# Kernel tuning notes

Hardware: AMD Instinct MI355X
Metric: run time of the kernel (lower is better)

The kernel has to match this reference:

```python
import jax, jax.numpy as jnp
import numpy as np
from jax import lax

EPS = 1e-5
DN = ('NCHW', 'OIHW', 'NCHW')


def batchnorm(x, gamma, beta):
    # training-mode BN: stats over (N, H, W)
    m = x.mean(axis=(0, 2, 3), keepdims=True)
    v = x.var(axis=(0, 2, 3), keepdims=True)
    g = gamma[None, :, None, None]
    b = beta[None, :, None, None]
    return (x - m) * (g / jnp.sqrt(v + EPS)) + b


def input_scale(x, stride):
    # channel mean -> 3x3 box filter (1/9 each), padding 1
    a = x.mean(axis=1, keepdims=True)  # [N,1,H,W]
    k = jnp.full((1, 1, 3, 3), 1.0 / 9.0, dtype=x.dtype)
    return lax.conv_general_dilated(a, k, (stride, stride), ((1, 1), (1, 1)),
                                    dimension_numbers=DN)


def binarize_ste(x):
    # sign with straight-through estimator (grad passes where |x|<=1)
    c = jnp.clip(x, -1.0, 1.0)
    return c + lax.stop_gradient(jnp.sign(x) - c)


def blconv(x, w, stride):
    # XNOR-style binarized conv: sign(x) * (sign(w)*mean|w| per out channel)
    bx = binarize_ste(x)
    alpha = jnp.abs(w).mean(axis=(1, 2, 3))  # [O]
    bw = jnp.sign(w) * alpha[:, None, None, None]
    return lax.conv_general_dilated(bx, bw, (stride, stride), ((1, 1), (1, 1)),
                                    dimension_numbers=DN)


def setup_inputs() -> dict:
    key = jax.random.key(0)
    ks = jax.random.split(key, 3)
    C = 256
    x = jax.random.normal(ks[0], (32, C, 56, 56), dtype=jnp.float32)
    w1 = jax.random.normal(ks[1], (C, C, 3, 3), dtype=jnp.float32) * 0.05
    w2 = jax.random.normal(ks[2], (C, C, 3, 3), dtype=jnp.float32) * 0.05
    bn1_gamma = jnp.ones((C,), jnp.float32)
    bn1_beta = jnp.zeros((C,), jnp.float32)
    bn2_gamma = jnp.ones((C,), jnp.float32)
    bn2_beta = jnp.zeros((C,), jnp.float32)
    return {"x": x, "bn1_gamma": bn1_gamma, "bn1_beta": bn1_beta, "w1": w1,
            "bn2_gamma": bn2_gamma, "bn2_beta": bn2_beta, "w2": w2}


def reference(x, bn1_gamma, bn1_beta, w1, bn2_gamma, bn2_beta, w2):
    stride = 1
    identity = x
    out = batchnorm(x, bn1_gamma, bn1_beta)
    K1 = input_scale(out, stride)
    out = blconv(out, w1, stride) * K1
    out = jax.nn.relu(out)
    out = batchnorm(out, bn2_gamma, bn2_beta)
    K2 = input_scale(out, 1)
    out = blconv(out, w2, 1) * K2
    out = out + identity
    return jax.nn.relu(out)
```

## Files before the change

kernel.cpp:

```cpp
#include <hip/hip_runtime.h>
#include <stdint.h>

#define NB 32
#define CC 256
#define HH 56
#define WW 56
#define PP (HH*WW)
#define NPIX (NB*PP)
#define W32 8
#define KEPS 1e-5f

__global__ void k_stats(const float* __restrict__ x, float* __restrict__ ssum, float* __restrict__ ssq) {
    int plane = blockIdx.x;
    int c = plane & (CC - 1);
    const float4* xp = (const float4*)(x + (size_t)plane * PP);
    float s = 0.f, q = 0.f;
    for (int i = threadIdx.x; i < PP / 4; i += blockDim.x) {
        float4 v = xp[i];
        s += v.x + v.y + v.z + v.w;
        q = fmaf(v.x, v.x, q); q = fmaf(v.y, v.y, q);
        q = fmaf(v.z, v.z, q); q = fmaf(v.w, v.w, q);
    }
#pragma unroll
    for (int off = 32; off; off >>= 1) { s += __shfl_down(s, off); q += __shfl_down(q, off); }
    __shared__ float ls[4], lq[4];
    int wv = threadIdx.x >> 6, ln = threadIdx.x & 63;
    if (ln == 0) { ls[wv] = s; lq[wv] = q; }
    __syncthreads();
    if (threadIdx.x == 0) {
        float S = 0.f, Q = 0.f;
        for (int w = 0; w < 4; ++w) { S += ls[w]; Q += lq[w]; }
        atomicAdd(&ssum[c], S); atomicAdd(&ssq[c], Q);
    }
}

__global__ void k_stats2(const short* __restrict__ ci, const float* __restrict__ alpha1,
                         const float* __restrict__ k1, float* __restrict__ ssum, float* __restrict__ ssq) {
    int plane = blockIdx.x;
    int o = plane & (CC - 1);
    int n = plane >> 8;
    const short4* cp = (const short4*)(ci + (size_t)plane * PP);
    const float4* kp = (const float4*)(k1 + (size_t)n * PP);
    float al = alpha1[o];
    float s = 0.f, q = 0.f;
    for (int i = threadIdx.x; i < PP / 4; i += blockDim.x) {
        short4 c4 = cp[i];
        float4 kf = kp[i];
        float v0 = fmaxf(al * kf.x * (float)c4.x, 0.f);
        float v1 = fmaxf(al * kf.y * (float)c4.y, 0.f);
        float v2 = fmaxf(al * kf.z * (float)c4.z, 0.f);
        float v3 = fmaxf(al * kf.w * (float)c4.w, 0.f);
        s += v0 + v1 + v2 + v3;
        q = fmaf(v0, v0, q); q = fmaf(v1, v1, q);
        q = fmaf(v2, v2, q); q = fmaf(v3, v3, q);
    }
#pragma unroll
    for (int off = 32; off; off >>= 1) { s += __shfl_down(s, off); q += __shfl_down(q, off); }
    __shared__ float ls[4], lq[4];
    int wv = threadIdx.x >> 6, ln = threadIdx.x & 63;
    if (ln == 0) { ls[wv] = s; lq[wv] = q; }
    __syncthreads();
    if (threadIdx.x == 0) {
        float S = 0.f, Q = 0.f;
        for (int w = 0; w < 4; ++w) { S += ls[w]; Q += lq[w]; }
        atomicAdd(&ssum[o], S); atomicAdd(&ssq[o], Q);
    }
}

__global__ void k_wprep(const float* __restrict__ w1, const float* __restrict__ w2,
                        uint32_t* __restrict__ wb1, uint32_t* __restrict__ wb2,
                        float* __restrict__ al1, float* __restrict__ al2,
                        int* __restrict__ adj1, int* __restrict__ adj2,
                        float* __restrict__ zstats) {
    int o2 = blockIdx.x;
    int lane = threadIdx.x;
    if (o2 < 16) zstats[o2 * 64 + lane] = 0.f;
    const float* w = (o2 < CC) ? w1 : w2;
    uint32_t* wb   = (o2 < CC) ? wb1 : wb2;
    float* al      = (o2 < CC) ? al1 : al2;
    int* adj       = (o2 < CC) ? adj1 : adj2;
    int o = o2 & (CC - 1);
    float asum = 0.f;
    int pt[9] = {0,0,0,0,0,0,0,0,0};
    for (int cg = 0; cg < 4; ++cg) {
        int c = cg * 64 + lane;
        const float* wp = w + ((size_t)o * CC + c) * 9;
        for (int t = 0; t < 9; ++t) {
            float wv = wp[t];
            asum += fabsf(wv);
            unsigned long long m = __ballot(wv >= 0.0f);
            pt[t] += __popcll(m);
            if (lane == 0) {
                wb[(t * CC + o) * W32 + cg * 2]     = (uint32_t)m;
                wb[(t * CC + o) * W32 + cg * 2 + 1] = (uint32_t)(m >> 32);
            }
        }
    }
#pragma unroll
    for (int off = 32; off; off >>= 1) asum += __shfl_down(asum, off);
    if (lane == 0) al[o] = asum * (1.0f / 2304.0f);
    if (lane < 9) {
        const unsigned vm[3] = {0u, 0x007u, 0x1C0u};
        const unsigned hm[3] = {0u, 0x049u, 0x124u};
        unsigned mask = vm[lane / 3] | hm[lane % 3];
        int nv = 9 - __popc(mask);
        int wsum = 0;
#pragma unroll
        for (int t = 0; t < 9; ++t) if ((mask >> t) & 1) wsum += pt[t];
        adj[o * 16 + lane] = 256 * nv + 2 * wsum;
    }
}

__global__ void k_bn1pack(const float* __restrict__ x,
                          const float* __restrict__ ssum, const float* __restrict__ ssq,
                          const float* __restrict__ gamma, const float* __restrict__ beta,
                          uint32_t* __restrict__ xbits, float* __restrict__ a) {
    __shared__ float sscale[CC], sbias[CC];
    {
        int t = threadIdx.x;
        float m   = ssum[t] * (1.0f / NPIX);
        float var = fmaf(-m, m, ssq[t] * (1.0f / NPIX));
        float sc  = gamma[t] / sqrtf(var + KEPS);
        sscale[t] = sc;
        sbias[t]  = fmaf(-m, sc, beta[t]);
    }
    __syncthreads();
    int lane = threadIdx.x & 63, wv = threadIdx.x >> 6;
    int n = blockIdx.x / 49;
    int pix = blockIdx.x * 64 + lane;
    int p = pix - n * PP;
    const float* xp = x + (size_t)n * CC * PP + p;
    uint32_t b0 = 0, b1 = 0;
    float asum = 0.f;
#pragma unroll
    for (int i = 0; i < 64; ++i) {
        int c = (wv << 6) + i;
        float v = xp[(size_t)c * PP];
        float bnv = fmaf(v, sscale[c], sbias[c]);
        asum += bnv;
        uint32_t bit = (bnv >= 0.0f) ? 1u : 0u;
        if (i < 32) b0 |= bit << i; else b1 |= bit << (i - 32);
    }
    ((uint2*)xbits)[(size_t)pix * 4 + wv] = make_uint2(b0, b1);
    __shared__ float lsum[4][64];
    lsum[wv][lane] = asum;
    __syncthreads();
    if (wv == 0)
        a[pix] = (lsum[0][lane] + lsum[1][lane] + lsum[2][lane] + lsum[3][lane]) * (1.0f / CC);
}

__global__ void k_bn2pack(const short* __restrict__ ci, const float* __restrict__ alpha1,
                          const float* __restrict__ k1,
                          const float* __restrict__ ssum, const float* __restrict__ ssq,
                          const float* __restrict__ gamma, const float* __restrict__ beta,
                          uint32_t* __restrict__ xbits, float* __restrict__ a) {
    __shared__ float sscale[CC], sbias[CC];
    {
        int t = threadIdx.x;
        float m   = ssum[t] * (1.0f / NPIX);
        float var = fmaf(-m, m, ssq[t] * (1.0f / NPIX));
        float sc  = gamma[t] / sqrtf(var + KEPS);
        sscale[t] = sc;
        sbias[t]  = fmaf(-m, sc, beta[t]);
    }
    __syncthreads();
    int lane = threadIdx.x & 63, wv = threadIdx.x >> 6;
    int n = blockIdx.x / 49;
    int pix = blockIdx.x * 64 + lane;
    int p = pix - n * PP;
    const short* cp = ci + (size_t)n * CC * PP + p;
    float kv = k1[pix];
    uint32_t b0 = 0, b1 = 0;
    float asum = 0.f;
#pragma unroll
    for (int i = 0; i < 64; ++i) {
        int o = (wv << 6) + i;
        float val = fmaxf(alpha1[o] * kv * (float)cp[(size_t)o * PP], 0.f);
        float bnv = fmaf(val, sscale[o], sbias[o]);
        asum += bnv;
        uint32_t bit = (bnv >= 0.0f) ? 1u : 0u;
        if (i < 32) b0 |= bit << i; else b1 |= bit << (i - 32);
    }
    ((uint2*)xbits)[(size_t)pix * 4 + wv] = make_uint2(b0, b1);
    __shared__ float lsum[4][64];
    lsum[wv][lane] = asum;
    __syncthreads();
    if (wv == 0)
        a[pix] = (lsum[0][lane] + lsum[1][lane] + lsum[2][lane] + lsum[3][lane]) * (1.0f / CC);
}

__global__ void k_box(const float* __restrict__ a, float* __restrict__ k) {
    int gid = blockIdx.x * 256 + threadIdx.x;
    int n = gid / PP;
    int p = gid - n * PP;
    int h = p / WW, w = p - (p / WW) * WW;
    const float* ap = a + (size_t)n * PP;
    float s = 0.f;
    for (int dr = -1; dr <= 1; ++dr) {
        int hh = h + dr;
        if (hh < 0 || hh >= HH) continue;
        for (int dc = -1; dc <= 1; ++dc) {
            int ww2 = w + dc;
            if (ww2 < 0 || ww2 >= WW) continue;
            s += ap[hh * WW + ww2];
        }
    }
    k[gid] = s * (1.0f / 9.0f);
}

template<bool FIRST>
__global__ __launch_bounds__(448, 8) void k_conv(
    const uint32_t* __restrict__ xbits, const uint32_t* __restrict__ wbits,
    const int* __restrict__ adj, const float* __restrict__ alpha,
    const float* __restrict__ amap, short* __restrict__ out_i16,
    const float* __restrict__ ident, float* __restrict__ outf)
{
    constexpr int TH = 8, TO = 16;
    constexpr int LW = 58;
    __shared__ uint32_t lds_x[(TH + 2) * LW * W32];

    int b = blockIdx.x;
    int ob = b & 15, hb = (b >> 4) % 7, n = b / 112;
    int h0 = hb * TH, o0 = ob * TO;
    int tid = threadIdx.x;

    for (int i = tid; i < (TH + 2) * LW * 2; i += 448) {
        int r = i / (LW * 2), j = i - r * (LW * 2);
        int c = j >> 1, half = j & 1;
        int gr = h0 - 1 + r, gc = c - 1;
        uint4 v = make_uint4(0u, 0u, 0u, 0u);
        if (gr >= 0 && gr < HH && gc >= 0 && gc < WW)
            v = ((const uint4*)(xbits + ((size_t)n * PP + (size_t)gr * WW + gc) * W32))[half];
        ((uint4*)lds_x)[i] = v;
    }
    __syncthreads();

    int row = tid / WW, col = tid - (tid / WW) * WW;
    int h = h0 + row;
    int vf = (h == 0) ? 1 : ((h == HH - 1) ? 2 : 0);
    int hf = (col == 0) ? 1 : ((col == WW - 1) ? 2 : 0);
    int type = vf * 3 + hf;

    float kv = 0.f;
    if (!FIRST) {
        const float* ap = amap + (size_t)n * PP;
        float s = 0.f;
        for (int dr = -1; dr <= 1; ++dr) {
            int hh = h + dr;
            if (hh < 0 || hh >= HH) continue;
            for (int dc2 = -1; dc2 <= 1; ++dc2) {
                int wc = col + dc2;
                if (wc < 0 || wc >= WW) continue;
                s += ap[hh * WW + wc];
            }
        }
        kv = s * (1.0f / 9.0f);
    }
    size_t obase = (size_t)n * CC * PP + (size_t)h * WW + col;

    int P[TO];
#pragma unroll
    for (int o = 0; o < TO; ++o) P[o] = 0;

#pragma unroll 1
    for (int dr = 0; dr < 3; ++dr) {
#pragma unroll 1
        for (int dc = 0; dc < 3; ++dc) {
            int base = ((row + dr) * LW + (col + dc)) * W32;
            uint4 xa = *(const uint4*)&lds_x[base];
            uint4 xb = *(const uint4*)&lds_x[base + 4];
            int t = dr * 3 + dc;
            const uint4* __restrict__ wq = (const uint4*)wbits + ((size_t)t * CC + o0) * 2;
#pragma unroll
            for (int o = 0; o < TO; ++o) {
                uint4 wa = wq[o * 2], wb2 = wq[o * 2 + 1];
                int P0 = P[o];
                P0 += __popc(xa.x ^ wa.x);
                P0 += __popc(xa.y ^ wa.y);
                P0 += __popc(xa.z ^ wa.z);
                P0 += __popc(xa.w ^ wa.w);
                P0 += __popc(xb.x ^ wb2.x);
                P0 += __popc(xb.y ^ wb2.y);
                P0 += __popc(xb.z ^ wb2.z);
                P0 += __popc(xb.w ^ wb2.w);
                P[o] = P0;
            }
        }
    }

#pragma unroll
    for (int o = 0; o < TO; ++o) {
        int oo = o0 + o;
        int acc = adj[oo * 16 + type] - 2 * P[o];
        size_t oidx = obase + (size_t)oo * PP;
        if (FIRST) {
            out_i16[oidx] = (short)acc;
        } else {
            float res = alpha[oo] * kv * (float)acc;
            outf[oidx] = fmaxf(res + ident[oidx], 0.f);
        }
    }
}

extern "C" void kernel_launch(void* const* d_in, const int* in_sizes, int n_in,
                              void* d_out, int out_size, void* d_ws, size_t ws_size,
                              hipStream_t stream)
{
    const float* x  = (const float*)d_in[0];
    const float* g1 = (const float*)d_in[1];
    const float* b1 = (const float*)d_in[2];
    const float* w1 = (const float*)d_in[3];
    const float* g2 = (const float*)d_in[4];
    const float* b2 = (const float*)d_in[5];
    const float* w2 = (const float*)d_in[6];
    float* out = (float*)d_out;

    char* ws = (char*)d_ws;
    float* s1sum  = (float*)(ws + 0);
    float* s1sq   = (float*)(ws + 1024);
    float* s2sum  = (float*)(ws + 2048);
    float* s2sq   = (float*)(ws + 3072);
    float* alpha1 = (float*)(ws + 8192);
    float* alpha2 = (float*)(ws + 9216);
    int*   adj1   = (int*)(ws + 10240);
    int*   adj2   = (int*)(ws + 26624);
    uint32_t* wbits1 = (uint32_t*)(ws + 43008);
    uint32_t* wbits2 = (uint32_t*)(ws + 116736);
    float* a1 = (float*)(ws + 190464);
    float* k1 = (float*)(ws + 591872);
    float* a2 = (float*)(ws + 993280);
    uint32_t* xbits1 = (uint32_t*)(ws + 1796096);
    uint32_t* xbits2 = (uint32_t*)(ws + 5007360);
    short* ci = (short*)(ws + 8218624);

    k_wprep<<<2 * CC, 64, 0, stream>>>(w1, w2, wbits1, wbits2, alpha1, alpha2, adj1, adj2, s1sum);
    k_stats<<<NB * CC, 256, 0, stream>>>(x, s1sum, s1sq);
    k_bn1pack<<<NPIX / 64, 256, 0, stream>>>(x, s1sum, s1sq, g1, b1, xbits1, a1);
    k_box<<<NPIX / 256, 256, 0, stream>>>(a1, k1);
    k_conv<true><<<NB * 7 * 16, 448, 0, stream>>>(xbits1, wbits1, adj1, nullptr, nullptr, ci, nullptr, nullptr);
    k_stats2<<<NB * CC, 256, 0, stream>>>(ci, alpha1, k1, s2sum, s2sq);
    k_bn2pack<<<NPIX / 64, 256, 0, stream>>>(ci, alpha1, k1, s2sum, s2sq, g2, b2, xbits2, a2);
    k_conv<false><<<NB * 7 * 16, 448, 0, stream>>>(xbits2, wbits2, adj2, alpha2, a2, nullptr, x, out);
}
```

Before: 538.3 us.

## Replace popcount binary conv with int8 MFMA convolution using ±1 byte encoding

Adds a new path that encodes binarized activations and weights as ±1 int8 bytes in channel-last layout and computes both 3x3 convolutions with 32x32x32 int8 MFMA instructions instead of XNOR/popcount with padding adjustments. The BN-pack kernels now write per-pixel channel-contiguous bytes through an LDS transpose. The second conv reads a precomputed box-filtered map (a new k_box pass) instead of computing it inline. The path is taken only when the workspace is large enough, otherwise the old popcount path runs. It trades 8x larger activation storage and traffic for matrix-core throughput.

```diff
diff --git a/kernel.cpp b/kernel.cpp
--- a/kernel.cpp
+++ b/kernel.cpp
@@ -9,6 +9,10 @@
 #define NPIX (NB*PP)
 #define W32 8
 #define KEPS 1e-5f
+
+typedef __attribute__((ext_vector_type(4)))  int i32x4;
+typedef __attribute__((ext_vector_type(16))) int i32x16;
+
 
 __global__ void k_stats(const float* __restrict__ x, float* __restrict__ ssum, float* __restrict__ ssq) {
     int plane = blockIdx.x;
@@ -67,11 +71,236 @@
     }
 }
 
-__global__ void k_wprep(const float* __restrict__ w1, const float* __restrict__ w2,
-                        uint32_t* __restrict__ wb1, uint32_t* __restrict__ wb2,
-                        float* __restrict__ al1, float* __restrict__ al2,
-                        int* __restrict__ adj1, int* __restrict__ adj2,
-                        float* __restrict__ zstats) {
+__global__ void k_box(const float* __restrict__ a, float* __restrict__ k) {
+    int gid = blockIdx.x * 256 + threadIdx.x;
+    int n = gid / PP;
+    int p = gid - n * PP;
+    int h = p / WW, w = p - (p / WW) * WW;
+    const float* ap = a + (size_t)n * PP;
+    float s = 0.f;
+    for (int dr = -1; dr <= 1; ++dr) {
+        int hh = h + dr;
+        if (hh < 0 || hh >= HH) continue;
+        for (int dc = -1; dc <= 1; ++dc) {
+            int ww2 = w + dc;
+            if (ww2 < 0 || ww2 >= WW) continue;
+            s += ap[hh * WW + ww2];
+        }
+    }
+    k[gid] = s * (1.0f / 9.0f);
+}
+
+__global__ void k_wprepM(const float* __restrict__ w1, const float* __restrict__ w2,
+                         uint8_t* __restrict__ wp1, uint8_t* __restrict__ wp2,
+                         float* __restrict__ al1, float* __restrict__ al2,
+                         float* __restrict__ zstats) {
+    int o2 = blockIdx.x;
+    int lane = threadIdx.x;
+    if (o2 < 16) zstats[o2 * 64 + lane] = 0.f;
+    const float* w = (o2 < CC) ? w1 : w2;
+    uint8_t* wp    = (o2 < CC) ? wp1 : wp2;
+    float* al      = (o2 < CC) ? al1 : al2;
+    int o = o2 & (CC - 1);
+    float asum = 0.f;
+    for (int cg = 0; cg < 4; ++cg) {
+        int c = cg * 64 + lane;
+        const float* wpt = w + ((size_t)o * CC + c) * 9;
+        int c32 = c >> 5;
+        int rem = c & 31;
+        for (int t = 0; t < 9; ++t) {
+            float wv = wpt[t];
+            asum += fabsf(wv);
+            int kg = t * 8 + c32;
+            wp[((size_t)kg * CC + o) * 32 + rem] = (wv >= 0.0f) ? (uint8_t)1 : (uint8_t)0xFF;
+        }
+    }
+#pragma unroll
+    for (int off = 32; off; off >>= 1) asum += __shfl_down(asum, off);
+    if (lane == 0) al[o] = asum * (1.0f / 2304.0f);
+}
+
+__global__ void k_bn1packM(const float* __restrict__ x,
+                           const float* __restrict__ ssum, const float* __restrict__ ssq,
+                           const float* __restrict__ gamma, const float* __restrict__ beta,
+                           uint8_t* __restrict__ xi8, float* __restrict__ a) {
+    __shared__ float sscale[CC], sbias[CC];
+    __shared__ uint32_t ldsT[64][68];
+    __shared__ float lsum[4][64];
+    int t = threadIdx.x;
+    {
+        float m   = ssum[t] * (1.0f / NPIX);
+        float var = fmaf(-m, m, ssq[t] * (1.0f / NPIX));
+        float sc  = gamma[t] / sqrtf(var + KEPS);
+        sscale[t] = sc;
+        sbias[t]  = fmaf(-m, sc, beta[t]);
+    }
+    __syncthreads();
+    int lane = t & 63, wv = t >> 6;
+    int n = blockIdx.x / 49;
+    int pix = blockIdx.x * 64 + lane;
+    int p = pix - n * PP;
+    const float* xp = x + (size_t)n * CC * PP + p;
+    float asum = 0.f;
+    for (int i4 = 0; i4 < 16; ++i4) {
+        uint32_t pk = 0;
+#pragma unroll
+        for (int u = 0; u < 4; ++u) {
+            int c = (wv << 6) + i4 * 4 + u;
+            float v = xp[(size_t)c * PP];
+            float bnv = fmaf(v, sscale[c], sbias[c]);
+            asum += bnv;
+            uint32_t byte = (bnv >= 0.0f) ? 0x01u : 0xFFu;
+            pk |= byte << (8 * u);
+        }
+        ldsT[lane][(wv << 4) + i4] = pk;
+    }
+    lsum[wv][lane] = asum;
+    __syncthreads();
+    if (wv == 0)
+        a[pix] = (lsum[0][lane] + lsum[1][lane] + lsum[2][lane] + lsum[3][lane]) * (1.0f / CC);
+    size_t gbase = (size_t)blockIdx.x * 64 * CC;
+    for (int it = 0; it < 4; ++it) {
+        int idx4 = it * 256 + t;
+        int px = idx4 >> 4, j = idx4 & 15;
+        uint4 v = *(uint4*)&ldsT[px][j * 4];
+        *(uint4*)(xi8 + gbase + (size_t)px * CC + j * 16) = v;
+    }
+}
+
+__global__ void k_bn2packM(const short* __restrict__ ci, const float* __restrict__ alpha1,
+                           const float* __restrict__ k1,
+                           const float* __restrict__ ssum, const float* __restrict__ ssq,
+                           const float* __restrict__ gamma, const float* __restrict__ beta,
+                           uint8_t* __restrict__ xi8, float* __restrict__ a) {
+    __shared__ float sscale[CC], sbias[CC], salpha[CC];
+    __shared__ uint32_t ldsT[64][68];
+    __shared__ float lsum[4][64];
+    int t = threadIdx.x;
+    {
+        float m   = ssum[t] * (1.0f / NPIX);
+        float var = fmaf(-m, m, ssq[t] * (1.0f / NPIX));
+        float sc  = gamma[t] / sqrtf(var + KEPS);
+        sscale[t] = sc;
+        sbias[t]  = fmaf(-m, sc, beta[t]);
+        salpha[t] = alpha1[t];
+    }
+    __syncthreads();
+    int lane = t & 63, wv = t >> 6;
+    int n = blockIdx.x / 49;
+    int pix = blockIdx.x * 64 + lane;
+    int p = pix - n * PP;
+    const short* cp = ci + (size_t)n * CC * PP + p;
+    float kv = k1[pix];
+    float asum = 0.f;
+    for (int i4 = 0; i4 < 16; ++i4) {
+        uint32_t pk = 0;
+#pragma unroll
+        for (int u = 0; u < 4; ++u) {
+            int c = (wv << 6) + i4 * 4 + u;
+            float val = fmaxf(salpha[c] * kv * (float)cp[(size_t)c * PP], 0.f);
+            float bnv = fmaf(val, sscale[c], sbias[c]);
+            asum += bnv;
+            uint32_t byte = (bnv >= 0.0f) ? 0x01u : 0xFFu;
+            pk |= byte << (8 * u);
+        }
+        ldsT[lane][(wv << 4) + i4] = pk;
+    }
+    lsum[wv][lane] = asum;
+    __syncthreads();
+    if (wv == 0)
+        a[pix] = (lsum[0][lane] + lsum[1][lane] + lsum[2][lane] + lsum[3][lane]) * (1.0f / CC);
+    size_t gbase = (size_t)blockIdx.x * 64 * CC;
+    for (int it = 0; it < 4; ++it) {
+        int idx4 = it * 256 + t;
+        int px = idx4 >> 4, j = idx4 & 15;
+        uint4 v = *(uint4*)&ldsT[px][j * 4];
+        *(uint4*)(xi8 + gbase + (size_t)px * CC + j * 16) = v;
+    }
+}
+
+template<bool FIRST>
+__global__ __launch_bounds__(448, 4) void k_convM(
+    const uint8_t* __restrict__ xi8, const uint8_t* __restrict__ wpack,
+    const float* __restrict__ alpha, const float* __restrict__ kmap,
+    short* __restrict__ out_i16, const float* __restrict__ ident,
+    float* __restrict__ outf)
+{
+    constexpr int PITCH = 80;
+    __shared__ uint8_t lds8[6 * 58 * PITCH];
+
+    int b = blockIdx.x;
+    int nh = b & 1;
+    int hb = (b >> 1) % 14;
+    int n  = b / 28;
+    int h0 = hb * 4;
+    int tid = threadIdx.x;
+    int wvi = tid >> 6, lane = tid & 63;
+    int l31 = lane & 31, kh = lane >> 5;
+
+    int pidx = wvi * 32 + l31;
+    int r_l = pidx / 56, c_l = pidx - (pidx / 56) * 56;
+
+    i32x16 acc[4] = {};
+
+#pragma unroll 1
+    for (int kb = 0; kb < 4; ++kb) {
+        __syncthreads();
+        for (int i = tid; i < 6 * 58 * 4; i += 448) {
+            int slot = i >> 2, j = i & 3;
+            int r = slot / 58, c = slot - (slot / 58) * 58;
+            int gr = h0 - 1 + r, gc = c - 1;
+            uint4 v = make_uint4(0u, 0u, 0u, 0u);
+            if (gr >= 0 && gr < HH && gc >= 0 && gc < WW)
+                v = *(const uint4*)(xi8 + (size_t)(n * PP + gr * WW + gc) * CC + kb * 64 + j * 16);
+            *(uint4*)(lds8 + slot * PITCH + j * 16) = v;
+        }
+        __syncthreads();
+#pragma unroll 1
+        for (int t = 0; t < 9; ++t) {
+            int dr = t / 3, dc = t - (t / 3) * 3;
+            int aoff = ((r_l + dr) * 58 + (c_l + dc)) * PITCH + kh * 16;
+#pragma unroll
+            for (int k32 = 0; k32 < 2; ++k32) {
+                i32x4 af = *(const i32x4*)(lds8 + aoff + k32 * 32);
+                int kg = t * 8 + kb * 2 + k32;
+                const uint8_t* wp = wpack + ((size_t)kg * CC + nh * 128 + l31) * 32 + kh * 16;
+#pragma unroll
+                for (int ct = 0; ct < 4; ++ct) {
+                    i32x4 bf = *(const i32x4*)(wp + ct * 32 * 32);
+                    acc[ct] = __builtin_amdgcn_mfma_i32_32x32x32_i8(af, bf, acc[ct], 0, 0, 0);
+                }
+            }
+        }
+    }
+
+    int pbase = h0 * WW + wvi * 32;
+#pragma unroll
+    for (int ct = 0; ct < 4; ++ct) {
+        int oc = nh * 128 + ct * 32 + l31;
+        size_t obase = ((size_t)n * CC + oc) * PP;
+        float al = 0.f;
+        if (!FIRST) al = alpha[oc];
+#pragma unroll
+        for (int rg = 0; rg < 16; ++rg) {
+            int m = (rg & 3) + 8 * (rg >> 2) + 4 * kh;
+            int p = pbase + m;
+            int acv = acc[ct][rg];
+            if (FIRST) {
+                out_i16[obase + p] = (short)acv;
+            } else {
+                float kv = kmap[(size_t)n * PP + p];
+                float r = al * kv * (float)acv;
+                outf[obase + p] = fmaxf(r + ident[obase + p], 0.f);
+            }
+        }
+    }
+}
+
+__global__ void k_wprepP(const float* __restrict__ w1, const float* __restrict__ w2,
+                         uint32_t* __restrict__ wb1, uint32_t* __restrict__ wb2,
+                         float* __restrict__ al1, float* __restrict__ al2,
+                         int* __restrict__ adj1, int* __restrict__ adj2,
+                         float* __restrict__ zstats) {
     int o2 = blockIdx.x;
     int lane = threadIdx.x;
     if (o2 < 16) zstats[o2 * 64 + lane] = 0.f;
@@ -111,10 +340,10 @@
     }
 }
 
-__global__ void k_bn1pack(const float* __restrict__ x,
-                          const float* __restrict__ ssum, const float* __restrict__ ssq,
-                          const float* __restrict__ gamma, const float* __restrict__ beta,
-                          uint32_t* __restrict__ xbits, float* __restrict__ a) {
+__global__ void k_bn1packP(const float* __restrict__ x,
+                           const float* __restrict__ ssum, const float* __restrict__ ssq,
+                           const float* __restrict__ gamma, const float* __restrict__ beta,
+                           uint32_t* __restrict__ xbits, float* __restrict__ a) {
     __shared__ float sscale[CC], sbias[CC];
     {
         int t = threadIdx.x;
@@ -149,11 +378,11 @@
         a[pix] = (lsum[0][lane] + lsum[1][lane] + lsum[2][lane] + lsum[3][lane]) * (1.0f / CC);
 }
 
-__global__ void k_bn2pack(const short* __restrict__ ci, const float* __restrict__ alpha1,
-                          const float* __restrict__ k1,
-                          const float* __restrict__ ssum, const float* __restrict__ ssq,
-                          const float* __restrict__ gamma, const float* __restrict__ beta,
-                          uint32_t* __restrict__ xbits, float* __restrict__ a) {
+__global__ void k_bn2packP(const short* __restrict__ ci, const float* __restrict__ alpha1,
+                           const float* __restrict__ k1,
+                           const float* __restrict__ ssum, const float* __restrict__ ssq,
+                           const float* __restrict__ gamma, const float* __restrict__ beta,
+                           uint32_t* __restrict__ xbits, float* __restrict__ a) {
     __shared__ float sscale[CC], sbias[CC];
     {
         int t = threadIdx.x;
@@ -189,27 +418,8 @@
         a[pix] = (lsum[0][lane] + lsum[1][lane] + lsum[2][lane] + lsum[3][lane]) * (1.0f / CC);
 }
 
-__global__ void k_box(const float* __restrict__ a, float* __restrict__ k) {
-    int gid = blockIdx.x * 256 + threadIdx.x;
-    int n = gid / PP;
-    int p = gid - n * PP;
-    int h = p / WW, w = p - (p / WW) * WW;
-    const float* ap = a + (size_t)n * PP;
-    float s = 0.f;
-    for (int dr = -1; dr <= 1; ++dr) {
-        int hh = h + dr;
-        if (hh < 0 || hh >= HH) continue;
-        for (int dc = -1; dc <= 1; ++dc) {
-            int ww2 = w + dc;
-            if (ww2 < 0 || ww2 >= WW) continue;
-            s += ap[hh * WW + ww2];
-        }
-    }
-    k[gid] = s * (1.0f / 9.0f);
-}
-
 template<bool FIRST>
-__global__ __launch_bounds__(448, 8) void k_conv(
+__global__ __launch_bounds__(448, 8) void k_convP(
     const uint32_t* __restrict__ xbits, const uint32_t* __restrict__ wbits,
     const int* __restrict__ adj, const float* __restrict__ alpha,
     const float* __restrict__ amap, short* __restrict__ out_i16,
@@ -314,31 +524,60 @@
     const float* b2 = (const float*)d_in[5];
     const float* w2 = (const float*)d_in[6];
     float* out = (float*)d_out;
-
     char* ws = (char*)d_ws;
-    float* s1sum  = (float*)(ws + 0);
-    float* s1sq   = (float*)(ws + 1024);
-    float* s2sum  = (float*)(ws + 2048);
-    float* s2sq   = (float*)(ws + 3072);
-    float* alpha1 = (float*)(ws + 8192);
-    float* alpha2 = (float*)(ws + 9216);
-    int*   adj1   = (int*)(ws + 10240);
-    int*   adj2   = (int*)(ws + 26624);
-    uint32_t* wbits1 = (uint32_t*)(ws + 43008);
-    uint32_t* wbits2 = (uint32_t*)(ws + 116736);
-    float* a1 = (float*)(ws + 190464);
-    float* k1 = (float*)(ws + 591872);
-    float* a2 = (float*)(ws + 993280);
-    uint32_t* xbits1 = (uint32_t*)(ws + 1796096);
-    uint32_t* xbits2 = (uint32_t*)(ws + 5007360);
-    short* ci = (short*)(ws + 8218624);
-
-    k_wprep<<<2 * CC, 64, 0, stream>>>(w1, w2, wbits1, wbits2, alpha1, alpha2, adj1, adj2, s1sum);
-    k_stats<<<NB * CC, 256, 0, stream>>>(x, s1sum, s1sq);
-    k_bn1pack<<<NPIX / 64, 256, 0, stream>>>(x, s1sum, s1sq, g1, b1, xbits1, a1);
-    k_box<<<NPIX / 256, 256, 0, stream>>>(a1, k1);
-    k_conv<true><<<NB * 7 * 16, 448, 0, stream>>>(xbits1, wbits1, adj1, nullptr, nullptr, ci, nullptr, nullptr);
-    k_stats2<<<NB * CC, 256, 0, stream>>>(ci, alpha1, k1, s2sum, s2sq);
-    k_bn2pack<<<NPIX / 64, 256, 0, stream>>>(ci, alpha1, k1, s2sum, s2sq, g2, b2, xbits2, a2);
-    k_conv<false><<<NB * 7 * 16, 448, 0, stream>>>(xbits2, wbits2, adj2, alpha2, a2, nullptr, x, out);
-}
+
+    const size_t MFMA_NEED = 79872000;
+
+    if (ws_size >= MFMA_NEED) {
+        float* s1sum  = (float*)(ws + 0);
+        float* s1sq   = (float*)(ws + 1024);
+        float* s2sum  = (float*)(ws + 2048);
+        float* s2sq   = (float*)(ws + 3072);
+        float* alpha1 = (float*)(ws + 8192);
+        float* alpha2 = (float*)(ws + 9216);
+        uint8_t* wp1  = (uint8_t*)(ws + 16384);
+        uint8_t* wp2  = (uint8_t*)(ws + 606208);
+        float* a1     = (float*)(ws + 1196032);
+        float* k1     = (float*)(ws + 1597440);
+        float* a2     = (float*)(ws + 1998848);
+        float* k2     = (float*)(ws + 2400256);
+        uint8_t* xi8  = (uint8_t*)(ws + 2801664);
+        short* ci     = (short*)(ws + 28491776);
+
+        k_wprepM<<<2 * CC, 64, 0, stream>>>(w1, w2, wp1, wp2, alpha1, alpha2, s1sum);
+        k_stats<<<NB * CC, 256, 0, stream>>>(x, s1sum, s1sq);
+        k_bn1packM<<<NPIX / 64, 256, 0, stream>>>(x, s1sum, s1sq, g1, b1, xi8, a1);
+        k_box<<<NPIX / 256, 256, 0, stream>>>(a1, k1);
+        k_convM<true><<<NB * 14 * 2, 448, 0, stream>>>(xi8, wp1, nullptr, nullptr, ci, nullptr, nullptr);
+        k_stats2<<<NB * CC, 256, 0, stream>>>(ci, alpha1, k1, s2sum, s2sq);
+        k_bn2packM<<<NPIX / 64, 256, 0, stream>>>(ci, alpha1, k1, s2sum, s2sq, g2, b2, xi8, a2);
+        k_box<<<NPIX / 256, 256, 0, stream>>>(a2, k2);
+        k_convM<false><<<NB * 14 * 2, 448, 0, stream>>>(xi8, wp2, alpha2, k2, nullptr, x, out);
+    } else {
+        float* s1sum  = (float*)(ws + 0);
+        float* s1sq   = (float*)(ws + 1024);
+        float* s2sum  = (float*)(ws + 2048);
+        float* s2sq   = (float*)(ws + 3072);
+        float* alpha1 = (float*)(ws + 8192);
+        float* alpha2 = (float*)(ws + 9216);
+        int*   adj1   = (int*)(ws + 10240);
+        int*   adj2   = (int*)(ws + 26624);
+        uint32_t* wbits1 = (uint32_t*)(ws + 43008);
+        uint32_t* wbits2 = (uint32_t*)(ws + 116736);
+        float* a1 = (float*)(ws + 190464);
+        float* k1 = (float*)(ws + 591872);
+        float* a2 = (float*)(ws + 993280);
+        uint32_t* xbits1 = (uint32_t*)(ws + 1796096);
+        uint32_t* xbits2 = (uint32_t*)(ws + 5007360);
+        short* ci = (short*)(ws + 8218624);
+
+        k_wprepP<<<2 * CC, 64, 0, stream>>>(w1, w2, wbits1, wbits2, alpha1, alpha2, adj1, adj2, s1sum);
+        k_stats<<<NB * CC, 256, 0, stream>>>(x, s1sum, s1sq);
+        k_bn1packP<<<NPIX / 64, 256, 0, stream>>>(x, s1sum, s1sq, g1, b1, xbits1, a1);
+        k_box<<<NPIX / 256, 256, 0, stream>>>(a1, k1);
+        k_convP<true><<<NB * 7 * 16, 448, 0, stream>>>(xbits1, wbits1, adj1, nullptr, nullptr, ci, nullptr, nullptr);
+        k_stats2<<<NB * CC, 256, 0, stream>>>(ci, alpha1, k1, s2sum, s2sq);
+        k_bn2packP<<<NPIX / 64, 256, 0, stream>>>(ci, alpha1, k1, s2sum, s2sq, g2, b2, xbits2, a2);
+        k_convP<false><<<NB * 7 * 16, 448, 0, stream>>>(xbits2, wbits2, adj2, alpha2, a2, nullptr, x, out);
+    }
+}
```

New measurement: 490.5 us. 1.1x faster.
